# Kernel optimization log

Measured on AMD Instinct MI355X. Metric: run time of the kernel, lower is better.

Reference implementation:

```python
import jax, jax.numpy as jnp
import numpy as np

N, E, F_IN, H, G, C = 100000, 1600000, 128, 128, 2048, 1
BN_EPS = 1e-5


def setup_inputs() -> dict:
    key = jax.random.key(0)
    ks = jax.random.split(key, 12)
    x = jax.random.normal(ks[0], (N, F_IN), dtype=jnp.float32)
    edge_index = jax.random.randint(ks[1], (2, E), 0, N, dtype=jnp.int64)
    batch = jnp.sort(jax.random.randint(ks[2], (N,), 0, G, dtype=jnp.int64))

    def xavier(k, fan_in, fan_out):
        lim = float(np.sqrt(6.0 / (fan_in + fan_out)))
        return jax.random.uniform(k, (fan_in, fan_out), jnp.float32, -lim, lim)

    return {
        "x": x, "edge_index": edge_index, "batch": batch,
        "W1": xavier(ks[3], F_IN, H), "b1": jnp.zeros((H,), jnp.float32),
        "g1": jnp.ones((H,), jnp.float32), "bt1": jnp.zeros((H,), jnp.float32),
        "W2": xavier(ks[4], H, H), "b2": jnp.zeros((H,), jnp.float32),
        "g2": jnp.ones((H,), jnp.float32), "bt2": jnp.zeros((H,), jnp.float32),
        "W3": xavier(ks[5], H, H), "b3": jnp.zeros((H,), jnp.float32),
        "g3": jnp.ones((H,), jnp.float32), "bt3": jnp.zeros((H,), jnp.float32),
        "fcw1": xavier(ks[6], H, H // 2), "fcb1": jnp.zeros((H // 2,), jnp.float32),
        "fcw2": xavier(ks[7], H // 2, C), "fcb2": jnp.zeros((C,), jnp.float32),
    }


def _gcn(x, W, b, src, dst, dis):
    # GCNConv: linear, then symmetric-normalized scatter-add with self-loops.
    xw = x @ W + b                                   # [N, H]
    norm = (dis[src] * dis[dst])[:, None]            # [E, 1]
    agg = jax.ops.segment_sum(xw[src] * norm, dst, num_segments=N)
    return agg + xw * (dis * dis)[:, None]           # self-loop term d^-1


def _bn(x, g, bt):
    mu = jnp.mean(x, axis=0)
    var = jnp.mean((x - mu) ** 2, axis=0)            # biased, training-mode BN
    return (x - mu) * jax.lax.rsqrt(var + BN_EPS) * g + bt


def reference(x, edge_index, batch, W1, b1, g1, bt1, W2, b2, g2, bt2,
              W3, b3, g3, bt3, fcw1, fcb1, fcw2, fcb2):
    src, dst = edge_index[0], edge_index[1]
    # degree with self-loops (counted on destination, as in PyG gcn_norm)
    deg = jax.ops.segment_sum(jnp.ones((E,), jnp.float32), dst, num_segments=N) + 1.0
    dis = jax.lax.rsqrt(deg)                         # deg^-1/2, deg >= 1

    h = jax.nn.relu(_bn(_gcn(x, W1, b1, src, dst, dis), g1, bt1))
    h = jax.nn.relu(_bn(_gcn(h, W2, b2, src, dst, dis), g2, bt2))
    h = jax.nn.relu(_bn(_gcn(h, W3, b3, src, dst, dis), g3, bt3))

    # global mean pool per graph
    sums = jax.ops.segment_sum(h, batch, num_segments=G)
    cnts = jax.ops.segment_sum(jnp.ones((N,), jnp.float32), batch, num_segments=G)
    pooled = sums / jnp.maximum(cnts, 1.0)[:, None]  # [G, H]

    out = jax.nn.relu(pooled @ fcw1 + fcb1)          # dropout is identity at eval
    return out @ fcw2 + fcb2                         # [G, C]
```

## Files before the change

kernel.cpp:

```cpp
#include <hip/hip_runtime.h>
#include <math.h>

#define Nn 100000
#define Ee 1600000
#define Gg 2048
#define HH 128
#define BN_EPS 1e-5f

#define NBK 196
#define NBLK_E 500
#define CHUNK4 800
#define NSTATB 256

typedef unsigned int uint32;
typedef unsigned short ushort_t;
typedef __attribute__((ext_vector_type(8))) short short8_t;
typedef __attribute__((ext_vector_type(8))) unsigned short ushort8_t;
typedef __attribute__((ext_vector_type(4))) float f32x4_t;

__device__ __forceinline__ ushort_t f2bf(float f) {
    union { float f; uint32 u; } c; c.f = f;
    uint32 r = (c.u + 0x7FFFu + ((c.u >> 16) & 1u)) >> 16;
    return (ushort_t)r;
}
__device__ __forceinline__ float bflo(uint32 v) {
    union { uint32 u; float f; } c; c.u = v << 16; return c.f;
}
__device__ __forceinline__ float bfhi(uint32 v) {
    union { uint32 u; float f; } c; c.u = v & 0xFFFF0000u; return c.f;
}

__global__ __launch_bounds__(256) void k_count(const int* __restrict__ dst,
                                               int* __restrict__ blkhist) {
    __shared__ unsigned h[NBK];
    int tid = threadIdx.x;
    for (int i = tid; i < NBK; i += 256) h[i] = 0;
    __syncthreads();
    const int4* d4 = (const int4*)dst + blockIdx.x * CHUNK4;
    for (int i = tid; i < CHUNK4; i += 256) {
        int4 v = d4[i];
        atomicAdd(&h[v.x >> 9], 1u);
        atomicAdd(&h[v.y >> 9], 1u);
        atomicAdd(&h[v.z >> 9], 1u);
        atomicAdd(&h[v.w >> 9], 1u);
    }
    __syncthreads();
    for (int i = tid; i < NBK; i += 256)
        blkhist[blockIdx.x * NBK + i] = (int)h[i];
}

__global__ __launch_bounds__(512) void k_bscan1(const int* __restrict__ blkhist,
                                                int* __restrict__ blkoff_rel,
                                                int* __restrict__ total) {
    __shared__ int tmp[512];
    int bucket = blockIdx.x;
    int t = threadIdx.x;
    int v = (t < NBLK_E) ? blkhist[t * NBK + bucket] : 0;
    tmp[t] = v;
    __syncthreads();
    for (int off = 1; off < 512; off <<= 1) {
        int u = (t >= off) ? tmp[t - off] : 0;
        __syncthreads();
        tmp[t] += u;
        __syncthreads();
    }
    if (t < NBLK_E) blkoff_rel[t * NBK + bucket] = tmp[t] - v;
    if (t == 511) total[bucket] = tmp[t];
}

__global__ void k_bscan2(const int* __restrict__ total,
                         int* __restrict__ bucket_base) {
    __shared__ int tmp[256];
    int t = threadIdx.x;
    int v = (t < NBK) ? total[t] : 0;
    tmp[t] = v;
    __syncthreads();
    for (int off = 1; off < 256; off <<= 1) {
        int u = (t >= off) ? tmp[t - off] : 0;
        __syncthreads();
        tmp[t] += u;
        __syncthreads();
    }
    if (t < NBK) bucket_base[t] = tmp[t] - v;
}

__global__ __launch_bounds__(256) void k_fill1(const int* __restrict__ src,
                                               const int* __restrict__ dst,
                                               const int* __restrict__ bucket_base,
                                               const int* __restrict__ blkoff_rel,
                                               uint32* __restrict__ pairs) {
    __shared__ int loff[NBK];
    __shared__ unsigned lh[NBK];
    int tid = threadIdx.x;
    for (int i = tid; i < NBK; i += 256) {
        loff[i] = bucket_base[i] + blkoff_rel[blockIdx.x * NBK + i];
        lh[i] = 0;
    }
    __syncthreads();
    const int4* s4 = (const int4*)src + blockIdx.x * CHUNK4;
    const int4* d4 = (const int4*)dst + blockIdx.x * CHUNK4;
    for (int i = tid; i < CHUNK4; i += 256) {
        int4 s = s4[i];
        int4 d = d4[i];
        int b0 = d.x >> 9; int r0 = (int)atomicAdd(&lh[b0], 1u);
        pairs[loff[b0] + r0] = ((uint32)(d.x & 511) << 17) | (uint32)s.x;
        int b1 = d.y >> 9; int r1 = (int)atomicAdd(&lh[b1], 1u);
        pairs[loff[b1] + r1] = ((uint32)(d.y & 511) << 17) | (uint32)s.y;
        int b2 = d.z >> 9; int r2 = (int)atomicAdd(&lh[b2], 1u);
        pairs[loff[b2] + r2] = ((uint32)(d.z & 511) << 17) | (uint32)s.z;
        int b3 = d.w >> 9; int r3 = (int)atomicAdd(&lh[b3], 1u);
        pairs[loff[b3] + r3] = ((uint32)(d.w & 511) << 17) | (uint32)s.w;
    }
}

__global__ __launch_bounds__(1024) void k_fill2(const int* __restrict__ bucket_base,
                                                const int* __restrict__ total,
                                                const uint32* __restrict__ pairs,
                                                int* __restrict__ csr_src,
                                                int* __restrict__ rowptr,
                                                float* __restrict__ dis) {
    __shared__ unsigned lcnt[512];
    __shared__ int tmp[512];
    __shared__ int lcur[512];
    int b = blockIdx.x;
    int node0 = b * 512;
    int tid = threadIdx.x;
    for (int i = tid; i < 512; i += 1024) lcnt[i] = 0;
    __syncthreads();
    int beg = bucket_base[b];
    int endp = beg + total[b];
    for (int j = beg + tid; j < endp; j += 1024)
        atomicAdd(&lcnt[pairs[j] >> 17], 1u);
    __syncthreads();
    if (tid < 512) tmp[tid] = (int)lcnt[tid];
    __syncthreads();
    for (int off = 1; off < 512; off <<= 1) {
        int u = (tid < 512 && tid >= off) ? tmp[tid - off] : 0;
        __syncthreads();
        if (tid < 512) tmp[tid] += u;
        __syncthreads();
    }
    if (tid < 512) {
        int excl = tmp[tid] - (int)lcnt[tid];
        int n = node0 + tid;
        if (n <= Nn) rowptr[n] = beg + excl;
        if (n < Nn) dis[n] = rsqrtf((float)lcnt[tid] + 1.0f);
        lcur[tid] = beg + excl;
    }
    __syncthreads();
    for (int j = beg + tid; j < endp; j += 1024) {
        uint32 p = pairs[j];
        int dl = (int)(p >> 17);
        int s = (int)(p & 0x1FFFFu);
        int pos = atomicAdd(&lcur[dl], 1);
        csr_src[pos] = s;
    }
}

__global__ __launch_bounds__(256) void k_wprep(const float* __restrict__ W1,
                                               const float* __restrict__ W2,
                                               const float* __restrict__ W3,
                                               ushort_t* __restrict__ Wb) {
    int l = blockIdx.x >> 6, part = blockIdx.x & 63;
    const float* W = (l == 0) ? W1 : (l == 1) ? W2 : W3;
    int i = part * 256 + threadIdx.x;
    int k = i >> 7, col = i & 127;
    Wb[l * 16384 + col * 128 + k] = f2bf(W[k * 128 + col]);
}

__global__ __launch_bounds__(256) void k_gemm(const float* __restrict__ Xf,
                                              const uint32* __restrict__ Xb,
                                              const ushort_t* __restrict__ Wb,
                                              const float* __restrict__ Bv,
                                              const float* __restrict__ bnp,
                                              const float* __restrict__ dis,
                                              ushort_t* __restrict__ XWb) {
    __shared__ ushort_t Wlds[128 * 136];
    __shared__ ushort_t Xlds[64 * 136];
    const int tid = threadIdx.x;
    const int rowbase = blockIdx.x * 64;

#pragma unroll
    for (int it = 0; it < 8; ++it) {
        int chunk = tid + it * 256;
        int col = chunk >> 4, kg = chunk & 15;
        *(ushort8_t*)&Wlds[col * 136 + kg * 8] =
            *(const ushort8_t*)&Wb[col * 128 + kg * 8];
    }
    {
        int row = tid >> 2, q = tid & 3;
        int g = rowbase + row;
        if (bnp == nullptr) {
            const float4* Xr = (const float4*)(Xf + (size_t)g * 128);
#pragma unroll
            for (int it = 0; it < 8; ++it) {
                int c4 = q + it * 4;
                float4 v;
                if (g < Nn) v = Xr[c4];
                else { v.x = v.y = v.z = v.w = 0.f; }
                ushort4 o;
                o.x = f2bf(v.x); o.y = f2bf(v.y); o.z = f2bf(v.z); o.w = f2bf(v.w);
                *(ushort4*)&Xlds[row * 136 + c4 * 4] = o;
            }
        } else {
            const uint4* Hr = (const uint4*)(Xb + (size_t)g * 64);
#pragma unroll
            for (int it = 0; it < 4; ++it) {
                int i4 = q + it * 4;
                int c0 = i4 * 8;
                ushort8_t o;
                if (g < Nn) {
                    uint4 u = Hr[i4];
                    float4 sca = *(const float4*)&bnp[c0];
                    float4 scb = *(const float4*)&bnp[c0 + 4];
                    float4 sha = *(const float4*)&bnp[128 + c0];
                    float4 shb = *(const float4*)&bnp[128 + c0 + 4];
                    o[0] = f2bf(fmaxf(fmaf(bflo(u.x), sca.x, sha.x), 0.f));
                    o[1] = f2bf(fmaxf(fmaf(bfhi(u.x), sca.y, sha.y), 0.f));
                    o[2] = f2bf(fmaxf(fmaf(bflo(u.y), sca.z, sha.z), 0.f));
                    o[3] = f2bf(fmaxf(fmaf(bfhi(u.y), sca.w, sha.w), 0.f));
                    o[4] = f2bf(fmaxf(fmaf(bflo(u.z), scb.x, shb.x), 0.f));
                    o[5] = f2bf(fmaxf(fmaf(bfhi(u.z), scb.y, shb.y), 0.f));
                    o[6] = f2bf(fmaxf(fmaf(bflo(u.w), scb.z, shb.z), 0.f));
                    o[7] = f2bf(fmaxf(fmaf(bfhi(u.w), scb.w, shb.w), 0.f));
                } else {
                    for (int j = 0; j < 8; ++j) o[j] = 0;
                }
                *(ushort8_t*)&Xlds[row * 136 + c0] = o;
            }
        }
    }
    __syncthreads();

    const int wid = tid >> 6, lane = tid & 63;
    const int arow = wid * 16 + (lane & 15);
    const int koff = (lane >> 4) * 8;
    const int bcol = lane & 15;

    f32x4_t acc[8];
#pragma unroll
    for (int nt = 0; nt < 8; ++nt) acc[nt] = (f32x4_t){0.f, 0.f, 0.f, 0.f};

#pragma unroll
    for (int kt = 0; kt < 4; ++kt) {
        short8_t a = *(const short8_t*)&Xlds[arow * 136 + kt * 32 + koff];
#pragma unroll
        for (int nt = 0; nt < 8; ++nt) {
            short8_t b = *(const short8_t*)&Wlds[(nt * 16 + bcol) * 136 + kt * 32 + koff];
            acc[nt] = __builtin_amdgcn_mfma_f32_16x16x32_bf16(a, b, acc[nt], 0, 0, 0);
        }
    }

    int er = wid * 16 + (lane >> 4) * 4;
    int r0 = rowbase + er;
    float dv[4];
#pragma unroll
    for (int i = 0; i < 4; ++i) dv[i] = (r0 + i < Nn) ? dis[r0 + i] : 0.f;
    __syncthreads();
#pragma unroll
    for (int nt = 0; nt < 8; ++nt) {
        int col = nt * 16 + bcol;
        float bs = Bv[col];
#pragma unroll
        for (int i = 0; i < 4; ++i)
            Xlds[(er + i) * 136 + col] = f2bf((acc[nt][i] + bs) * dv[i]);
    }
    __syncthreads();
#pragma unroll
    for (int it = 0; it < 4; ++it) {
        int chunk = tid + it * 256;
        int row = chunk >> 4, cg = chunk & 15;
        int g = rowbase + row;
        if (g < Nn)
            *(uint4*)&XWb[(size_t)g * 128 + cg * 8] =
                *(const uint4*)&Xlds[row * 136 + cg * 8];
    }
}

__global__ __launch_bounds__(256) void k_agg(const uint32* __restrict__ XW32,
                                             const float* __restrict__ dis,
                                             const int* __restrict__ rowptr,
                                             const int* __restrict__ csr_src,
                                             uint32* __restrict__ HP32) {
    __shared__ int sidx[256];
    int w = threadIdx.x >> 6;
    int lane = threadIdx.x & 63;
    int half = lane >> 5, li = lane & 31;
    int node = (blockIdx.x * 4 + w) * 2 + half;
    const uint2* XW64 = (const uint2*)XW32;
    int beg = rowptr[node], end = rowptr[node + 1];
    int* widx = &sidx[w * 64];
    float a0 = 0.f, a1 = 0.f, a2 = 0.f, a3 = 0.f;
    int base = beg;
    while (__any(base < end)) {
        int j = base + li;
        if (j < end) widx[lane] = csr_src[j];
        __builtin_amdgcn_wave_barrier();
        int m = end - base; m = (m > 32) ? 32 : m;
        int k = 0;
        for (; k + 8 <= m; k += 8) {
            int s0 = widx[half * 32 + k + 0];
            int s1 = widx[half * 32 + k + 1];
            int s2 = widx[half * 32 + k + 2];
            int s3 = widx[half * 32 + k + 3];
            int s4 = widx[half * 32 + k + 4];
            int s5 = widx[half * 32 + k + 5];
            int s6 = widx[half * 32 + k + 6];
            int s7 = widx[half * 32 + k + 7];
            uint2 v0 = XW64[(size_t)s0 * 32 + li];
            uint2 v1 = XW64[(size_t)s1 * 32 + li];
            uint2 v2 = XW64[(size_t)s2 * 32 + li];
            uint2 v3 = XW64[(size_t)s3 * 32 + li];
            uint2 v4 = XW64[(size_t)s4 * 32 + li];
            uint2 v5 = XW64[(size_t)s5 * 32 + li];
            uint2 v6 = XW64[(size_t)s6 * 32 + li];
            uint2 v7 = XW64[(size_t)s7 * 32 + li];
            a0 += bflo(v0.x); a1 += bfhi(v0.x); a2 += bflo(v0.y); a3 += bfhi(v0.y);
            a0 += bflo(v1.x); a1 += bfhi(v1.x); a2 += bflo(v1.y); a3 += bfhi(v1.y);
            a0 += bflo(v2.x); a1 += bfhi(v2.x); a2 += bflo(v2.y); a3 += bfhi(v2.y);
            a0 += bflo(v3.x); a1 += bfhi(v3.x); a2 += bflo(v3.y); a3 += bfhi(v3.y);
            a0 += bflo(v4.x); a1 += bfhi(v4.x); a2 += bflo(v4.y); a3 += bfhi(v4.y);
            a0 += bflo(v5.x); a1 += bfhi(v5.x); a2 += bflo(v5.y); a3 += bfhi(v5.y);
            a0 += bflo(v6.x); a1 += bfhi(v6.x); a2 += bflo(v6.y); a3 += bfhi(v6.y);
            a0 += bflo(v7.x); a1 += bfhi(v7.x); a2 += bflo(v7.y); a3 += bfhi(v7.y);
        }
        for (; k < m; ++k) {
            int s = widx[half * 32 + k];
            uint2 v = XW64[(size_t)s * 32 + li];
            a0 += bflo(v.x); a1 += bfhi(v.x); a2 += bflo(v.y); a3 += bfhi(v.y);
        }
        base += 32;
        __builtin_amdgcn_wave_barrier();
    }
    uint2 vs = XW64[(size_t)node * 32 + li];
    a0 += bflo(vs.x); a1 += bfhi(vs.x); a2 += bflo(vs.y); a3 += bfhi(vs.y);
    float d = dis[node];
    uint2 r;
    r.x = (uint32)f2bf(a0 * d) | ((uint32)f2bf(a1 * d) << 16);
    r.y = (uint32)f2bf(a2 * d) | ((uint32)f2bf(a3 * d) << 16);
    ((uint2*)HP32)[(size_t)node * 32 + li] = r;
}

__global__ __launch_bounds__(256) void k_statsA(const uint32* __restrict__ HP32,
                                                float* __restrict__ partials) {
    const uint2* HPu2 = (const uint2*)HP32;
    int tid = threadIdx.x;
    int li = tid & 31;
    int s  = tid >> 5;
    float s0 = 0.f, s1 = 0.f, s2 = 0.f, s3 = 0.f;
    float q0 = 0.f, q1 = 0.f, q2 = 0.f, q3 = 0.f;
    for (int r = blockIdx.x * 8 + s; r < Nn; r += NSTATB * 8) {
        uint2 v = HPu2[(size_t)r * 32 + li];
        float a = bflo(v.x), b = bfhi(v.x), c = bflo(v.y), d = bfhi(v.y);
        s0 += a; s1 += b; s2 += c; s3 += d;
        q0 = fmaf(a, a, q0); q1 = fmaf(b, b, q1);
        q2 = fmaf(c, c, q2); q3 = fmaf(d, d, q3);
    }
    __shared__ float arr[8 * 256];
    float* mine = &arr[s * 256 + li * 4];
    mine[0] = s0; mine[1] = s1; mine[2] = s2; mine[3] = s3;
    mine[128] = q0; mine[129] = q1; mine[130] = q2; mine[131] = q3;
    __syncthreads();
    float tot = 0.f;
#pragma unroll
    for (int k = 0; k < 8; ++k) tot += arr[k * 256 + tid];
    partials[blockIdx.x * 256 + tid] = tot;
}

__global__ __launch_bounds__(1024) void k_statsB(const float* __restrict__ partials,
                                                 const float* __restrict__ g,
                                                 const float* __restrict__ bt,
                                                 float* __restrict__ bnp) {
    int tid = threadIdx.x;
    int sub = tid >> 8;
    int t = tid & 255;
    float acc = 0.f;
#pragma unroll 8
    for (int r = sub * 64; r < sub * 64 + 64; ++r)
        acc += partials[r * 256 + t];
    __shared__ float red[4 * 256];
    red[sub * 256 + t] = acc;
    __syncthreads();
    __shared__ float tot[256];
    if (tid < 256)
        tot[tid] = red[tid] + red[256 + tid] + red[512 + tid] + red[768 + tid];
    __syncthreads();
    if (tid < 128) {
        float mu  = tot[tid] * (1.0f / Nn);
        float var = tot[128 + tid] * (1.0f / Nn) - mu * mu;
        float sc  = g[tid] * rsqrtf(var + BN_EPS);
        bnp[tid]       = sc;
        bnp[128 + tid] = bt[tid] - mu * sc;
    }
}

__global__ __launch_bounds__(128) void k_pool_fc(const ushort_t* __restrict__ HP16,
                                                 const float* __restrict__ bnp,
                                                 const int* __restrict__ batch,
                                                 const float* __restrict__ fcw1,
                                                 const float* __restrict__ fcb1,
                                                 const float* __restrict__ fcw2,
                                                 const float* __restrict__ fcb2,
                                                 float* __restrict__ out) {
    int g = blockIdx.x;
    int t = threadIdx.x;
    int lo = 0, hi = Nn;
    while (lo < hi) { int mid = (lo + hi) >> 1; if (batch[mid] < g) lo = mid + 1; else hi = mid; }
    int start = lo;
    hi = Nn;
    while (lo < hi) { int mid = (lo + hi) >> 1; if (batch[mid] < g + 1) lo = mid + 1; else hi = mid; }
    int end = lo;

    float sc = bnp[t], sh = bnp[128 + t];
    float acc = 0.f;
    for (int i = start; i < end; ++i) {
        union { uint32 u; float f; } c;
        c.u = (uint32)HP16[(size_t)i * 128 + t] << 16;
        acc += fmaxf(fmaf(c.f, sc, sh), 0.f);
    }
    float inv = 1.0f / fmaxf((float)(end - start), 1.0f);

    __shared__ float p[128];
    __shared__ float h1[64];
    p[t] = acc * inv;
    __syncthreads();
    if (t < 64) {
        float s = fcb1[t];
        for (int k = 0; k < 128; ++k) s = fmaf(p[k], fcw1[k * 64 + t], s);
        h1[t] = fmaxf(s, 0.f);
    }
    __syncthreads();
    if (t < 64) {
        float v = h1[t] * fcw2[t];
        for (int off = 32; off > 0; off >>= 1) v += __shfl_down(v, off, 64);
        if (t == 0) out[g] = v + fcb2[0];
    }
}

extern "C" void kernel_launch(void* const* d_in, const int* in_sizes, int n_in,
                              void* d_out, int out_size, void* d_ws, size_t ws_size,
                              hipStream_t stream) {
    const float* x     = (const float*)d_in[0];
    const int*   ei    = (const int*)d_in[1];
    const int*   batch = (const int*)d_in[2];
    const float* W1  = (const float*)d_in[3];
    const float* b1  = (const float*)d_in[4];
    const float* g1  = (const float*)d_in[5];
    const float* bt1 = (const float*)d_in[6];
    const float* W2  = (const float*)d_in[7];
    const float* b2  = (const float*)d_in[8];
    const float* g2  = (const float*)d_in[9];
    const float* bt2 = (const float*)d_in[10];
    const float* W3  = (const float*)d_in[11];
    const float* b3  = (const float*)d_in[12];
    const float* g3  = (const float*)d_in[13];
    const float* bt3 = (const float*)d_in[14];
    const float* fcw1 = (const float*)d_in[15];
    const float* fcb1 = (const float*)d_in[16];
    const float* fcw2 = (const float*)d_in[17];
    const float* fcb2 = (const float*)d_in[18];
    float* out = (float*)d_out;

    ushort_t* XWb     = (ushort_t*)d_ws;
    uint32*   HP32    = (uint32*)(XWb + (size_t)Nn * HH);
    float*    dis     = (float*)(HP32 + (size_t)Nn * 64);
    int*      rowptr  = (int*)(dis + Nn);
    int*      blkhist = rowptr + (Nn + 1);
    int*      blkoff_rel = blkhist + NBLK_E * NBK;
    int*      total   = blkoff_rel + NBLK_E * NBK;
    int*      bucket_base = total + NBK;
    uint32*   pairs   = (uint32*)(bucket_base + NBK);
    int*      csr_src = (int*)(pairs + Ee);
    float*    partials = (float*)(csr_src + Ee);
    float*    bnp     = partials + NSTATB * 256;
    ushort_t* Wb      = (ushort_t*)(bnp + 768);

    const int* src = ei;
    const int* dst = ei + Ee;

    k_count<<<NBLK_E, 256, 0, stream>>>(dst, blkhist);
    k_wprep<<<192, 256, 0, stream>>>(W1, W2, W3, Wb);
    k_bscan1<<<NBK, 512, 0, stream>>>(blkhist, blkoff_rel, total);
    k_bscan2<<<1, 256, 0, stream>>>(total, bucket_base);
    k_fill1<<<NBLK_E, 256, 0, stream>>>(src, dst, bucket_base, blkoff_rel, pairs);
    k_fill2<<<NBK, 1024, 0, stream>>>(bucket_base, total, pairs, csr_src, rowptr, dis);

    const float* bs_[3]  = {b1, b2, b3};
    const float* gs_[3]  = {g1, g2, g3};
    const float* bts_[3] = {bt1, bt2, bt3};
    const int ngemm = (Nn + 63) / 64;
    for (int l = 0; l < 3; ++l) {
        const float* bnp_in = (l == 0) ? nullptr : (bnp + (l - 1) * 256);
        k_gemm<<<ngemm, 256, 0, stream>>>(x, HP32, Wb + l * 16384, bs_[l], bnp_in, dis, XWb);
        k_agg<<<12500, 256, 0, stream>>>((const uint32*)XWb, dis, rowptr, csr_src, HP32);
        k_statsA<<<NSTATB, 256, 0, stream>>>(HP32, partials);
        k_statsB<<<1, 1024, 0, stream>>>(partials, gs_[l], bts_[l], bnp + l * 256);
    }
    k_pool_fc<<<Gg, 128, 0, stream>>>((const ushort_t*)HP32, bnp + 512, batch,
                                      fcw1, fcb1, fcw2, fcb2, out);
}
```

Before: 361.7 us.

## Quantize GEMM output to int8 with per-row scales to halve aggregation gathers

The GEMM epilogue now computes a per-row absolute maximum with a wave shuffle reduction. It writes XW as symmetric int8 with one float scale per source row, instead of bf16. The aggregation kernel stages (source index, scale) pairs in shared memory and gathers 4-byte int8 words in place of 8-byte bf16 pairs, dequantizing with an FMA. This is meant to halve the random-gather traffic that dominates the edge aggregation. In exchange it adds one scale load per edge, loses precision in the features, and drops the explicit 8-way unroll of the gather loop, which may reduce memory-level parallelism.

Result: faster. 311.1 us (-14.0%).

```diff
diff --git a/kernel.cpp b/kernel.cpp
--- a/kernel.cpp
+++ b/kernel.cpp
@@ -13,6 +13,7 @@
 #define NSTATB 256
 
 typedef unsigned int uint32;
+typedef unsigned char uchar_t;
 typedef unsigned short ushort_t;
 typedef __attribute__((ext_vector_type(8))) short short8_t;
 typedef __attribute__((ext_vector_type(8))) unsigned short ushort8_t;
@@ -28,6 +29,11 @@
 }
 __device__ __forceinline__ float bfhi(uint32 v) {
     union { uint32 u; float f; } c; c.u = v & 0xFFFF0000u; return c.f;
+}
+__device__ __forceinline__ int q8(float f, float inv) {
+    float t = f * inv;
+    t = fmaxf(fminf(t, 127.f), -127.f);
+    return (int)rintf(t);
 }
 
 __global__ __launch_bounds__(256) void k_count(const int* __restrict__ dst,
@@ -174,9 +180,11 @@
                                               const float* __restrict__ Bv,
                                               const float* __restrict__ bnp,
                                               const float* __restrict__ dis,
-                                              ushort_t* __restrict__ XWb) {
+                                              uchar_t* __restrict__ XW8,
+                                              float* __restrict__ sc_src) {
     __shared__ ushort_t Wlds[128 * 136];
     __shared__ ushort_t Xlds[64 * 136];
+    __shared__ float smax[64];
     const int tid = threadIdx.x;
     const int rowbase = blockIdx.x * 64;
 
@@ -257,13 +265,25 @@
 #pragma unroll
     for (int i = 0; i < 4; ++i) dv[i] = (r0 + i < Nn) ? dis[r0 + i] : 0.f;
     __syncthreads();
-#pragma unroll
-    for (int nt = 0; nt < 8; ++nt) {
-        int col = nt * 16 + bcol;
-        float bs = Bv[col];
-#pragma unroll
-        for (int i = 0; i < 4; ++i)
-            Xlds[(er + i) * 136 + col] = f2bf((acc[nt][i] + bs) * dv[i]);
+    float bs[8];
+#pragma unroll
+    for (int nt = 0; nt < 8; ++nt) bs[nt] = Bv[nt * 16 + bcol];
+    float rmax[4];
+#pragma unroll
+    for (int i = 0; i < 4; ++i) {
+        float m = 0.f;
+#pragma unroll
+        for (int nt = 0; nt < 8; ++nt) {
+            float v = (acc[nt][i] + bs[nt]) * dv[i];
+            m = fmaxf(m, fabsf(v));
+            Xlds[(er + i) * 136 + nt * 16 + bcol] = f2bf(v);
+        }
+        m = fmaxf(m, __shfl_xor(m, 1));
+        m = fmaxf(m, __shfl_xor(m, 2));
+        m = fmaxf(m, __shfl_xor(m, 4));
+        m = fmaxf(m, __shfl_xor(m, 8));
+        rmax[i] = m;
+        if (bcol == 0) smax[er + i] = m;
     }
     __syncthreads();
 #pragma unroll
@@ -271,69 +291,78 @@
         int chunk = tid + it * 256;
         int row = chunk >> 4, cg = chunk & 15;
         int g = rowbase + row;
-        if (g < Nn)
-            *(uint4*)&XWb[(size_t)g * 128 + cg * 8] =
-                *(const uint4*)&Xlds[row * 136 + cg * 8];
+        if (g < Nn) {
+            float mx = smax[row];
+            float inv = (mx > 0.f) ? (127.0f / mx) : 0.f;
+            uint4 u = *(const uint4*)&Xlds[row * 136 + cg * 8];
+            int b0 = q8(bflo(u.x), inv), b1 = q8(bfhi(u.x), inv);
+            int b2 = q8(bflo(u.y), inv), b3 = q8(bfhi(u.y), inv);
+            int b4 = q8(bflo(u.z), inv), b5 = q8(bfhi(u.z), inv);
+            int b6 = q8(bflo(u.w), inv), b7 = q8(bfhi(u.w), inv);
+            uint2 o;
+            o.x = (uint32)(b0 & 255) | ((uint32)(b1 & 255) << 8) |
+                  ((uint32)(b2 & 255) << 16) | ((uint32)(b3 & 255) << 24);
+            o.y = (uint32)(b4 & 255) | ((uint32)(b5 & 255) << 8) |
+                  ((uint32)(b6 & 255) << 16) | ((uint32)(b7 & 255) << 24);
+            *(uint2*)&XW8[(size_t)g * 128 + cg * 8] = o;
+            if (cg == 0) sc_src[g] = mx * (1.0f / 127.0f);
+        }
     }
 }
 
 __global__ __launch_bounds__(256) void k_agg(const uint32* __restrict__ XW32,
+                                             const float* __restrict__ sc_src,
                                              const float* __restrict__ dis,
                                              const int* __restrict__ rowptr,
                                              const int* __restrict__ csr_src,
                                              uint32* __restrict__ HP32) {
-    __shared__ int sidx[256];
+    __shared__ uint2 spair[256];
     int w = threadIdx.x >> 6;
     int lane = threadIdx.x & 63;
     int half = lane >> 5, li = lane & 31;
     int node = (blockIdx.x * 4 + w) * 2 + half;
-    const uint2* XW64 = (const uint2*)XW32;
     int beg = rowptr[node], end = rowptr[node + 1];
-    int* widx = &sidx[w * 64];
+    uint2* wpair = &spair[w * 64];
     float a0 = 0.f, a1 = 0.f, a2 = 0.f, a3 = 0.f;
     int base = beg;
     while (__any(base < end)) {
         int j = base + li;
-        if (j < end) widx[lane] = csr_src[j];
+        if (j < end) {
+            int s = csr_src[j];
+            float sc = sc_src[s];
+            uint2 p; p.x = (uint32)s; p.y = __float_as_uint(sc);
+            wpair[lane] = p;
+        }
         __builtin_amdgcn_wave_barrier();
         int m = end - base; m = (m > 32) ? 32 : m;
-        int k = 0;
-        for (; k + 8 <= m; k += 8) {
-            int s0 = widx[half * 32 + k + 0];
-            int s1 = widx[half * 32 + k + 1];
-            int s2 = widx[half * 32 + k + 2];
-            int s3 = widx[half * 32 + k + 3];
-            int s4 = widx[half * 32 + k + 4];
-            int s5 = widx[half * 32 + k + 5];
-            int s6 = widx[half * 32 + k + 6];
-            int s7 = widx[half * 32 + k + 7];
-            uint2 v0 = XW64[(size_t)s0 * 32 + li];
-            uint2 v1 = XW64[(size_t)s1 * 32 + li];
-            uint2 v2 = XW64[(size_t)s2 * 32 + li];
-            uint2 v3 = XW64[(size_t)s3 * 32 + li];
-            uint2 v4 = XW64[(size_t)s4 * 32 + li];
-            uint2 v5 = XW64[(size_t)s5 * 32 + li];
-            uint2 v6 = XW64[(size_t)s6 * 32 + li];
-            uint2 v7 = XW64[(size_t)s7 * 32 + li];
-            a0 += bflo(v0.x); a1 += bfhi(v0.x); a2 += bflo(v0.y); a3 += bfhi(v0.y);
-            a0 += bflo(v1.x); a1 += bfhi(v1.x); a2 += bflo(v1.y); a3 += bfhi(v1.y);
-            a0 += bflo(v2.x); a1 += bfhi(v2.x); a2 += bflo(v2.y); a3 += bfhi(v2.y);
-            a0 += bflo(v3.x); a1 += bfhi(v3.x); a2 += bflo(v3.y); a3 += bfhi(v3.y);
-            a0 += bflo(v4.x); a1 += bfhi(v4.x); a2 += bflo(v4.y); a3 += bfhi(v4.y);
-            a0 += bflo(v5.x); a1 += bfhi(v5.x); a2 += bflo(v5.y); a3 += bfhi(v5.y);
-            a0 += bflo(v6.x); a1 += bfhi(v6.x); a2 += bflo(v6.y); a3 += bfhi(v6.y);
-            a0 += bflo(v7.x); a1 += bfhi(v7.x); a2 += bflo(v7.y); a3 += bfhi(v7.y);
-        }
-        for (; k < m; ++k) {
-            int s = widx[half * 32 + k];
-            uint2 v = XW64[(size_t)s * 32 + li];
-            a0 += bflo(v.x); a1 += bfhi(v.x); a2 += bflo(v.y); a3 += bfhi(v.y);
+        for (int k = 0; k < m; ++k) {
+            uint2 p = wpair[half * 32 + k];
+            uint32 u = XW32[(size_t)p.x * 32 + li];
+            float sc = __uint_as_float(p.y);
+            int b0 = (int)(u << 24) >> 24;
+            int b1 = (int)(u << 16) >> 24;
+            int b2 = (int)(u << 8) >> 24;
+            int b3 = (int)u >> 24;
+            a0 = fmaf((float)b0, sc, a0);
+            a1 = fmaf((float)b1, sc, a1);
+            a2 = fmaf((float)b2, sc, a2);
+            a3 = fmaf((float)b3, sc, a3);
         }
         base += 32;
         __builtin_amdgcn_wave_barrier();
     }
-    uint2 vs = XW64[(size_t)node * 32 + li];
-    a0 += bflo(vs.x); a1 += bfhi(vs.x); a2 += bflo(vs.y); a3 += bfhi(vs.y);
+    {
+        uint32 u = XW32[(size_t)node * 32 + li];
+        float sc = sc_src[node];
+        int b0 = (int)(u << 24) >> 24;
+        int b1 = (int)(u << 16) >> 24;
+        int b2 = (int)(u << 8) >> 24;
+        int b3 = (int)u >> 24;
+        a0 = fmaf((float)b0, sc, a0);
+        a1 = fmaf((float)b1, sc, a1);
+        a2 = fmaf((float)b2, sc, a2);
+        a3 = fmaf((float)b3, sc, a3);
+    }
     float d = dis[node];
     uint2 r;
     r.x = (uint32)f2bf(a0 * d) | ((uint32)f2bf(a1 * d) << 16);
@@ -461,9 +490,10 @@
     const float* fcb2 = (const float*)d_in[18];
     float* out = (float*)d_out;
 
-    ushort_t* XWb     = (ushort_t*)d_ws;
-    uint32*   HP32    = (uint32*)(XWb + (size_t)Nn * HH);
-    float*    dis     = (float*)(HP32 + (size_t)Nn * 64);
+    uchar_t*  XW8     = (uchar_t*)d_ws;
+    uint32*   HP32    = (uint32*)(XW8 + (size_t)Nn * HH);
+    float*    sc_src  = (float*)(HP32 + (size_t)Nn * 64);
+    float*    dis     = sc_src + Nn;
     int*      rowptr  = (int*)(dis + Nn);
     int*      blkhist = rowptr + (Nn + 1);
     int*      blkoff_rel = blkhist + NBLK_E * NBK;
@@ -491,8 +521,10 @@
     const int ngemm = (Nn + 63) / 64;
     for (int l = 0; l < 3; ++l) {
         const float* bnp_in = (l == 0) ? nullptr : (bnp + (l - 1) * 256);
-        k_gemm<<<ngemm, 256, 0, stream>>>(x, HP32, Wb + l * 16384, bs_[l], bnp_in, dis, XWb);
-        k_agg<<<12500, 256, 0, stream>>>((const uint32*)XWb, dis, rowptr, csr_src, HP32);
+        k_gemm<<<ngemm, 256, 0, stream>>>(x, HP32, Wb + l * 16384, bs_[l], bnp_in,
+                                          dis, XW8, sc_src);
+        k_agg<<<12500, 256, 0, stream>>>((const uint32*)XW8, sc_src, dis, rowptr,
+                                         csr_src, HP32);
         k_statsA<<<NSTATB, 256, 0, stream>>>(HP32, partials);
         k_statsB<<<1, 1024, 0, stream>>>(partials, gs_[l], bts_[l], bnp + l * 256);
     }
```
